# Performance work log

Measured on AMD Instinct MI355X. Metric: run time of the kernel, lower is better.

Reference implementation:

```python
import jax, jax.numpy as jnp
import numpy as np

H = 128      # hidden_size
B = 8192     # number of sessions
L = 50       # items per session (constant here; code supports ragged)
T = B * L    # total tokens


def setup_inputs() -> dict:
    key = jax.random.key(0)
    ks = jax.random.split(key, 10)
    s = 1.0 / np.sqrt(H)
    u = lambda k, shape: jax.random.uniform(k, shape, jnp.float32, -s, s)
    return {
        "intra_item_emb": jax.random.normal(ks[0], (T, H), jnp.float32),
        "inter_item_emb": jax.random.normal(ks[1], (T, H), jnp.float32),
        "W1": u(ks[2], (H, H)), "b1": u(ks[3], (H,)),
        "W2": u(ks[4], (H, H)), "b2": u(ks[5], (H,)),
        "q_w": u(ks[6], (1, H)), "q_b": u(ks[7], (1,)),
        "W3": u(ks[8], (H, 2 * H)), "b3": u(ks[9], (H,)),
        "seq_len": jnp.full((B,), L, dtype=jnp.int32),
    }


def reference(intra_item_emb, inter_item_emb, W1, b1, W2, b2, q_w, q_b, W3, b3, seq_len):
    # max_fusing: elementwise max of the two embedding streams  [T, H]
    hidden = jnp.maximum(intra_item_emb, inter_item_emb)
    nB = seq_len.shape[0]
    nT = hidden.shape[0]
    # segment id per token and index of last token of each session
    seg_ids = jnp.repeat(jnp.arange(nB), seq_len, total_repeat_length=nT)  # [T]
    last_idx = jnp.cumsum(seq_len) - 1                                      # [B]
    v_n = hidden[last_idx]                 # [B, H] last node of each session
    v_n_rep = v_n[seg_ids]                 # [T, H] broadcast last node to tokens
    # attention weight per token: q(sigmoid(W1 v_n + W2 h))  [T, 1]
    alpha = jax.nn.sigmoid(v_n_rep @ W1.T + b1 + hidden @ W2.T + b2) @ q_w.T + q_b
    # segment-sum pooling of alpha-weighted tokens  [B, H]
    s_g = jax.ops.segment_sum(alpha * hidden, seg_ids, num_segments=nB)
    # final session representation  [B, H]
    h_s = jnp.concatenate([v_n, s_g], axis=1) @ W3.T + b3
    return h_s
```

## Files before the change

kernel.cpp:

```cpp
#include <hip/hip_runtime.h>
#include <hip/hip_bf16.h>

#define HDIM 128
#define RS 136

typedef __attribute__((ext_vector_type(8))) short short8;
typedef __attribute__((ext_vector_type(4))) float floatv4;

static __device__ __forceinline__ unsigned short f2bf(float f) {
  union { float f; unsigned u; } x; x.f = f;
  unsigned r = x.u + 0x7fffu + ((x.u >> 16) & 1u);
  return (unsigned short)(r >> 16);
}
static __device__ __forceinline__ float blo(unsigned u) { return __uint_as_float(u << 16); }
static __device__ __forceinline__ float bhi(unsigned u) { return __uint_as_float(u & 0xffff0000u); }

__global__ void prep_kernel(const int* __restrict__ seq, int* __restrict__ offs, int B,
                            const float* __restrict__ W1, const float* __restrict__ W2,
                            const float* __restrict__ W3,
                            unsigned short* __restrict__ w1b, unsigned short* __restrict__ w2b,
                            unsigned short* __restrict__ w3b) {
  if (blockIdx.x == 0) {
    __shared__ int part[256];
    int tid = threadIdx.x;
    int chunk = (B + 255) >> 8;
    int beg = tid * chunk, end = min(beg + chunk, B);
    int s = 0;
    for (int i = beg; i < end; ++i) s += seq[i];
    part[tid] = s;
    __syncthreads();
    for (int d = 1; d < 256; d <<= 1) {
      int v = (tid >= d) ? part[tid - d] : 0;
      __syncthreads();
      part[tid] += v;
      __syncthreads();
    }
    int run = (tid == 0) ? 0 : part[tid - 1];
    for (int i = beg; i < end; ++i) { offs[i] = run; run += seq[i]; }
  } else {
    int i = (blockIdx.x - 1) * 256 + threadIdx.x;
    if (i < 16384) { w1b[i] = f2bf(W1[i]); w2b[i] = f2bf(W2[i]); }
    if (i < 32768) { w3b[i] = f2bf(W3[i]); }
  }
}

__global__ __launch_bounds__(256) void session_kernel(
    const float* __restrict__ intra, const float* __restrict__ inter,
    const unsigned short* __restrict__ w1b, const float* __restrict__ b1,
    const unsigned short* __restrict__ w2b, const float* __restrict__ b2,
    const float* __restrict__ qw, const float* __restrict__ qb,
    const unsigned short* __restrict__ w3b, const float* __restrict__ b3,
    const int* __restrict__ seq, const int* __restrict__ offs,
    float* __restrict__ out) {
  __shared__ unsigned short hbf[64 * RS];
  __shared__ unsigned short vnb[HDIM];
  __shared__ unsigned short sgb[HDIM];
  __shared__ float alphaAcc[64];
  __shared__ float sgpart[4][HDIM];

  const int b = blockIdx.x;
  const int tid = threadIdx.x;
  const int lane = tid & 63, wid = tid >> 6;
  const int quad = lane >> 4, lcol = lane & 15;
  const int nbase = wid << 5;
  const int n0 = nbase + lcol, n1 = n0 + 16;

  int n = seq[b];
  const int start = offs[b];
  if (n > 64) n = 64;

  if (tid < HDIM) {
    int last = start + n - 1;
    if (last < 0) last = 0;
    size_t base = (size_t)last * HDIM + tid;
    vnb[tid] = f2bf(fmaxf(intra[base], inter[base]));
  }
  if (tid < 64) alphaAcc[tid] = qb[0];

  {
    const float4* pa = (const float4*)(intra + (size_t)start * HDIM);
    const float4* pb = (const float4*)(inter + (size_t)start * HDIM);
    #pragma unroll
    for (int it = 0; it < 8; ++it) {
      int idx = (it << 8) + tid;
      int t = idx >> 5, j4 = idx & 31;
      float4 r; r.x = 0.f; r.y = 0.f; r.z = 0.f; r.w = 0.f;
      if (t < n) {
        float4 a = pa[idx], c = pb[idx];
        r.x = fmaxf(a.x, c.x); r.y = fmaxf(a.y, c.y);
        r.z = fmaxf(a.z, c.z); r.w = fmaxf(a.w, c.w);
      }
      union { __hip_bfloat162 b; unsigned u; } p01, p23;
      p01.b = __float22bfloat162_rn(make_float2(r.x, r.y));
      p23.b = __float22bfloat162_rn(make_float2(r.z, r.w));
      uint2 st; st.x = p01.u; st.y = p23.u;
      *(uint2*)&hbf[t * RS + (j4 << 2)] = st;
    }
  }

  short8 w2f[2][4];
  #pragma unroll
  for (int nt = 0; nt < 2; ++nt) {
    int nn = nbase + (nt << 4) + lcol;
    #pragma unroll
    for (int kt = 0; kt < 4; ++kt)
      w2f[nt][kt] = *(const short8*)(w2b + nn * HDIM + (kt << 5) + (quad << 3));
  }
  __syncthreads();

  float c0, c1;
  {
    floatv4 p0 = {0.f, 0.f, 0.f, 0.f}, p1 = {0.f, 0.f, 0.f, 0.f};
    #pragma unroll
    for (int kt = 0; kt < 4; ++kt) {
      short8 af = *(const short8*)&vnb[(kt << 5) + (quad << 3)];
      short8 bf0 = *(const short8*)(w1b + n0 * HDIM + (kt << 5) + (quad << 3));
      short8 bf1 = *(const short8*)(w1b + n1 * HDIM + (kt << 5) + (quad << 3));
      p0 = __builtin_amdgcn_mfma_f32_16x16x32_bf16(af, bf0, p0, 0, 0, 0);
      p1 = __builtin_amdgcn_mfma_f32_16x16x32_bf16(af, bf1, p1, 0, 0, 0);
    }
    c0 = p0[0] + b1[n0] + b2[n0];
    c1 = p1[0] + b1[n1] + b2[n1];
  }
  const float q0 = qw[n0], q1 = qw[n1];

  #pragma unroll
  for (int mt = 0; mt < 4; ++mt) {
    floatv4 a0 = {c0, c0, c0, c0}, a1 = {c1, c1, c1, c1};
    const unsigned short* arow = &hbf[((mt << 4) + lcol) * RS + (quad << 3)];
    #pragma unroll
    for (int kt = 0; kt < 4; ++kt) {
      short8 af = *(const short8*)(arow + (kt << 5));
      a0 = __builtin_amdgcn_mfma_f32_16x16x32_bf16(af, w2f[0][kt], a0, 0, 0, 0);
      a1 = __builtin_amdgcn_mfma_f32_16x16x32_bf16(af, w2f[1][kt], a1, 0, 0, 0);
    }
    #pragma unroll
    for (int r = 0; r < 4; ++r) {
      float v = q0 * __builtin_amdgcn_rcpf(1.f + __expf(-a0[r]))
              + q1 * __builtin_amdgcn_rcpf(1.f + __expf(-a1[r]));
      v += __shfl_xor(v, 1, 64);
      v += __shfl_xor(v, 2, 64);
      v += __shfl_xor(v, 4, 64);
      v += __shfl_xor(v, 8, 64);
      if (lcol == 0) atomicAdd(&alphaAcc[(mt << 4) + (quad << 2) + r], v);
    }
  }
  __syncthreads();

  {
    int jg = tid & 15, ts = tid >> 4;
    float ac[8];
    #pragma unroll
    for (int e = 0; e < 8; ++e) ac[e] = 0.f;
    #pragma unroll
    for (int tt = 0; tt < 4; ++tt) {
      int t = (tt << 4) + ts;
      float al = alphaAcc[t];
      uint4 u = *(const uint4*)&hbf[t * RS + (jg << 3)];
      ac[0] += al * blo(u.x); ac[1] += al * bhi(u.x);
      ac[2] += al * blo(u.y); ac[3] += al * bhi(u.y);
      ac[4] += al * blo(u.z); ac[5] += al * bhi(u.z);
      ac[6] += al * blo(u.w); ac[7] += al * bhi(u.w);
    }
    #pragma unroll
    for (int e = 0; e < 8; ++e) {
      ac[e] += __shfl_xor(ac[e], 16, 64);
      ac[e] += __shfl_xor(ac[e], 32, 64);
    }
    if (quad == 0) {
      float4 s0; s0.x = ac[0]; s0.y = ac[1]; s0.z = ac[2]; s0.w = ac[3];
      float4 s1; s1.x = ac[4]; s1.y = ac[5]; s1.z = ac[6]; s1.w = ac[7];
      *(float4*)&sgpart[wid][(jg << 3)] = s0;
      *(float4*)&sgpart[wid][(jg << 3) + 4] = s1;
    }
  }
  __syncthreads();
  if (tid < HDIM) {
    float s = sgpart[0][tid] + sgpart[1][tid] + sgpart[2][tid] + sgpart[3][tid];
    sgb[tid] = f2bf(s);
  }
  __syncthreads();

  {
    floatv4 o0 = {0.f, 0.f, 0.f, 0.f}, o1 = {0.f, 0.f, 0.f, 0.f};
    #pragma unroll
    for (int kt = 0; kt < 8; ++kt) {
      const unsigned short* src = (kt < 4) ? &vnb[kt << 5] : &sgb[(kt - 4) << 5];
      short8 af = *(const short8*)(src + (quad << 3));
      short8 bf0 = *(const short8*)(w3b + n0 * 256 + (kt << 5) + (quad << 3));
      short8 bf1 = *(const short8*)(w3b + n1 * 256 + (kt << 5) + (quad << 3));
      o0 = __builtin_amdgcn_mfma_f32_16x16x32_bf16(af, bf0, o0, 0, 0, 0);
      o1 = __builtin_amdgcn_mfma_f32_16x16x32_bf16(af, bf1, o1, 0, 0, 0);
    }
    if (quad == 0) {
      out[(size_t)b * HDIM + n0] = o0[0] + b3[n0];
      out[(size_t)b * HDIM + n1] = o1[0] + b3[n1];
    }
  }
}

extern "C" void kernel_launch(void* const* d_in, const int* in_sizes, int n_in,
                              void* d_out, int out_size, void* d_ws, size_t ws_size,
                              hipStream_t stream) {
  const float* intra = (const float*)d_in[0];
  const float* inter = (const float*)d_in[1];
  const float* W1 = (const float*)d_in[2];
  const float* b1 = (const float*)d_in[3];
  const float* W2 = (const float*)d_in[4];
  const float* b2 = (const float*)d_in[5];
  const float* qw = (const float*)d_in[6];
  const float* qb = (const float*)d_in[7];
  const float* W3 = (const float*)d_in[8];
  const float* b3 = (const float*)d_in[9];
  const int* seq = (const int*)d_in[10];
  const int B = in_sizes[10];
  float* out = (float*)d_out;

  char* ws = (char*)d_ws;
  size_t o1 = (((size_t)B * 4) + 255) & ~(size_t)255;
  int* offs = (int*)ws;
  unsigned short* w1b = (unsigned short*)(ws + o1);
  unsigned short* w2b = (unsigned short*)(ws + o1 + 32768);
  unsigned short* w3b = (unsigned short*)(ws + o1 + 65536);

  hipLaunchKernelGGL(prep_kernel, dim3(129), dim3(256), 0, stream,
                     seq, offs, B, W1, W2, W3, w1b, w2b, w3b);
  hipLaunchKernelGGL(session_kernel, dim3(B), dim3(256), 0, stream,
                     intra, inter, w1b, b1, w2b, b2, qw, qb, w3b, b3, seq, offs, out);
}
```

Baseline: 507.6 us.

## Process eight sessions per block with register-prefetched next session loads

Each block now handles eight sessions. The next session's embeddings are prefetched into registers while the current one is being processed, which overlaps global loads with MFMA work. The W1 and W3 projections are batched across the eight sessions into single MFMA tiles, where before each block used one useful row out of sixteen. W2 fragments are loaded once per block instead of once per session. The cost is heavy register use for the prefetch buffers (launch bounds set to 3 blocks), one eighth as many blocks, and more syncs per block.

```diff
diff --git a/kernel.cpp b/kernel.cpp
--- a/kernel.cpp
+++ b/kernel.cpp
@@ -3,6 +3,8 @@
 
 #define HDIM 128
 #define RS 136
+#define XS 264
+#define SPB 8
 
 typedef __attribute__((ext_vector_type(8))) short short8;
 typedef __attribute__((ext_vector_type(4))) float floatv4;
@@ -44,140 +46,184 @@
   }
 }
 
-__global__ __launch_bounds__(256) void session_kernel(
+__global__ __launch_bounds__(256, 3) void session_kernel(
     const float* __restrict__ intra, const float* __restrict__ inter,
     const unsigned short* __restrict__ w1b, const float* __restrict__ b1,
     const unsigned short* __restrict__ w2b, const float* __restrict__ b2,
     const float* __restrict__ qw, const float* __restrict__ qb,
     const unsigned short* __restrict__ w3b, const float* __restrict__ b3,
     const int* __restrict__ seq, const int* __restrict__ offs,
-    float* __restrict__ out) {
+    float* __restrict__ out, int B) {
   __shared__ unsigned short hbf[64 * RS];
-  __shared__ unsigned short vnb[HDIM];
-  __shared__ unsigned short sgb[HDIM];
-  __shared__ float alphaAcc[64];
+  __shared__ unsigned short X[16 * XS];
+  __shared__ float cbuf[SPB][HDIM];
+  __shared__ float alphaPart[4][64];
   __shared__ float sgpart[4][HDIM];
 
-  const int b = blockIdx.x;
   const int tid = threadIdx.x;
   const int lane = tid & 63, wid = tid >> 6;
   const int quad = lane >> 4, lcol = lane & 15;
-  const int nbase = wid << 5;
-  const int n0 = nbase + lcol, n1 = n0 + 16;
-
-  int n = seq[b];
-  const int start = offs[b];
-  if (n > 64) n = 64;
-
-  if (tid < HDIM) {
-    int last = start + n - 1;
-    if (last < 0) last = 0;
-    size_t base = (size_t)last * HDIM + tid;
-    vnb[tid] = f2bf(fmaxf(intra[base], inter[base]));
-  }
-  if (tid < 64) alphaAcc[tid] = qb[0];
-
+  const int n0 = (wid << 5) + lcol, n1 = n0 + 16;
+  const int sid0 = blockIdx.x * SPB;
+
+  int n_nxt = 0, start_nxt = 0;
+  if (sid0 < B) { n_nxt = seq[sid0]; start_nxt = offs[sid0]; }
+
+  float4 ra[8], rb[8];
   {
-    const float4* pa = (const float4*)(intra + (size_t)start * HDIM);
-    const float4* pb = (const float4*)(inter + (size_t)start * HDIM);
+    const float4* pa = (const float4*)(intra + (size_t)start_nxt * HDIM);
+    const float4* pb = (const float4*)(inter + (size_t)start_nxt * HDIM);
+    int nc = (n_nxt > 64) ? 64 : n_nxt;
     #pragma unroll
     for (int it = 0; it < 8; ++it) {
       int idx = (it << 8) + tid;
-      int t = idx >> 5, j4 = idx & 31;
-      float4 r; r.x = 0.f; r.y = 0.f; r.z = 0.f; r.w = 0.f;
-      if (t < n) {
-        float4 a = pa[idx], c = pb[idx];
-        r.x = fmaxf(a.x, c.x); r.y = fmaxf(a.y, c.y);
-        r.z = fmaxf(a.z, c.z); r.w = fmaxf(a.w, c.w);
-      }
-      union { __hip_bfloat162 b; unsigned u; } p01, p23;
-      p01.b = __float22bfloat162_rn(make_float2(r.x, r.y));
-      p23.b = __float22bfloat162_rn(make_float2(r.z, r.w));
-      uint2 st; st.x = p01.u; st.y = p23.u;
-      *(uint2*)&hbf[t * RS + (j4 << 2)] = st;
-    }
-  }
+      int t = idx >> 5;
+      float4 va = {0.f, 0.f, 0.f, 0.f}, vb = {0.f, 0.f, 0.f, 0.f};
+      if (t < nc) { va = pa[idx]; vb = pb[idx]; }
+      ra[it] = va; rb[it] = vb;
+    }
+  }
+  if (1 < SPB && sid0 + 1 < B) { n_nxt = seq[sid0 + 1]; start_nxt = offs[sid0 + 1]; }
+  else { n_nxt = 0; start_nxt = 0; }
 
   short8 w2f[2][4];
   #pragma unroll
   for (int nt = 0; nt < 2; ++nt) {
-    int nn = nbase + (nt << 4) + lcol;
+    int nn = n0 + (nt << 4);
     #pragma unroll
     for (int kt = 0; kt < 4; ++kt)
       w2f[nt][kt] = *(const short8*)(w2b + nn * HDIM + (kt << 5) + (quad << 3));
   }
+  const float q0 = qw[n0], q1 = qw[n1];
+  const float sq = qb[0];
+
+  #pragma unroll
+  for (int it = 0; it < 4; ++it) {
+    int s = (it << 1) + (tid >> 7);
+    int col = tid & 127;
+    int sid = sid0 + s;
+    int ns = 0, st = 0;
+    if (sid < B) { ns = seq[sid]; st = offs[sid]; }
+    float v = 0.f;
+    if (ns > 0) {
+      size_t base = (size_t)(st + ns - 1) * HDIM + col;
+      v = fmaxf(intra[base], inter[base]);
+    }
+    X[s * XS + col] = f2bf(v);
+  }
   __syncthreads();
 
-  float c0, c1;
   {
     floatv4 p0 = {0.f, 0.f, 0.f, 0.f}, p1 = {0.f, 0.f, 0.f, 0.f};
     #pragma unroll
     for (int kt = 0; kt < 4; ++kt) {
-      short8 af = *(const short8*)&vnb[(kt << 5) + (quad << 3)];
+      short8 af = *(const short8*)&X[lcol * XS + (kt << 5) + (quad << 3)];
       short8 bf0 = *(const short8*)(w1b + n0 * HDIM + (kt << 5) + (quad << 3));
       short8 bf1 = *(const short8*)(w1b + n1 * HDIM + (kt << 5) + (quad << 3));
       p0 = __builtin_amdgcn_mfma_f32_16x16x32_bf16(af, bf0, p0, 0, 0, 0);
       p1 = __builtin_amdgcn_mfma_f32_16x16x32_bf16(af, bf1, p1, 0, 0, 0);
     }
-    c0 = p0[0] + b1[n0] + b2[n0];
-    c1 = p1[0] + b1[n1] + b2[n1];
-  }
-  const float q0 = qw[n0], q1 = qw[n1];
-
-  #pragma unroll
-  for (int mt = 0; mt < 4; ++mt) {
-    floatv4 a0 = {c0, c0, c0, c0}, a1 = {c1, c1, c1, c1};
-    const unsigned short* arow = &hbf[((mt << 4) + lcol) * RS + (quad << 3)];
-    #pragma unroll
-    for (int kt = 0; kt < 4; ++kt) {
-      short8 af = *(const short8*)(arow + (kt << 5));
-      a0 = __builtin_amdgcn_mfma_f32_16x16x32_bf16(af, w2f[0][kt], a0, 0, 0, 0);
-      a1 = __builtin_amdgcn_mfma_f32_16x16x32_bf16(af, w2f[1][kt], a1, 0, 0, 0);
-    }
-    #pragma unroll
-    for (int r = 0; r < 4; ++r) {
-      float v = q0 * __builtin_amdgcn_rcpf(1.f + __expf(-a0[r]))
-              + q1 * __builtin_amdgcn_rcpf(1.f + __expf(-a1[r]));
-      v += __shfl_xor(v, 1, 64);
-      v += __shfl_xor(v, 2, 64);
-      v += __shfl_xor(v, 4, 64);
-      v += __shfl_xor(v, 8, 64);
-      if (lcol == 0) atomicAdd(&alphaAcc[(mt << 4) + (quad << 2) + r], v);
+    if (quad < 2) {
+      float bb0 = b1[n0] + b2[n0], bb1 = b1[n1] + b2[n1];
+      #pragma unroll
+      for (int r = 0; r < 4; ++r) {
+        int m = (quad << 2) + r;
+        cbuf[m][n0] = p0[r] + bb0;
+        cbuf[m][n1] = p1[r] + bb1;
+      }
     }
   }
   __syncthreads();
 
-  {
-    int jg = tid & 15, ts = tid >> 4;
-    float ac[8];
-    #pragma unroll
-    for (int e = 0; e < 8; ++e) ac[e] = 0.f;
-    #pragma unroll
-    for (int tt = 0; tt < 4; ++tt) {
-      int t = (tt << 4) + ts;
-      float al = alphaAcc[t];
-      uint4 u = *(const uint4*)&hbf[t * RS + (jg << 3)];
-      ac[0] += al * blo(u.x); ac[1] += al * bhi(u.x);
-      ac[2] += al * blo(u.y); ac[3] += al * bhi(u.y);
-      ac[4] += al * blo(u.z); ac[5] += al * bhi(u.z);
-      ac[6] += al * blo(u.w); ac[7] += al * bhi(u.w);
-    }
-    #pragma unroll
-    for (int e = 0; e < 8; ++e) {
-      ac[e] += __shfl_xor(ac[e], 16, 64);
-      ac[e] += __shfl_xor(ac[e], 32, 64);
-    }
-    if (quad == 0) {
-      float4 s0; s0.x = ac[0]; s0.y = ac[1]; s0.z = ac[2]; s0.w = ac[3];
-      float4 s1; s1.x = ac[4]; s1.y = ac[5]; s1.z = ac[6]; s1.w = ac[7];
-      *(float4*)&sgpart[wid][(jg << 3)] = s0;
-      *(float4*)&sgpart[wid][(jg << 3) + 4] = s1;
-    }
-  }
-  __syncthreads();
-  if (tid < HDIM) {
-    float s = sgpart[0][tid] + sgpart[1][tid] + sgpart[2][tid] + sgpart[3][tid];
-    sgb[tid] = f2bf(s);
+  #pragma unroll 1
+  for (int s = 0; s < SPB; ++s) {
+    #pragma unroll
+    for (int it = 0; it < 8; ++it) {
+      int idx = (it << 8) + tid;
+      int t = idx >> 5, j4 = idx & 31;
+      float4 a = ra[it], c = rb[it];
+      union { __hip_bfloat162 b; unsigned u; } p01, p23;
+      p01.b = __float22bfloat162_rn(make_float2(fmaxf(a.x, c.x), fmaxf(a.y, c.y)));
+      p23.b = __float22bfloat162_rn(make_float2(fmaxf(a.z, c.z), fmaxf(a.w, c.w)));
+      uint2 st; st.x = p01.u; st.y = p23.u;
+      *(uint2*)&hbf[t * RS + (j4 << 2)] = st;
+    }
+    __syncthreads();
+
+    if (s + 1 < SPB) {
+      const float4* pa = (const float4*)(intra + (size_t)start_nxt * HDIM);
+      const float4* pb = (const float4*)(inter + (size_t)start_nxt * HDIM);
+      int nc = (n_nxt > 64) ? 64 : n_nxt;
+      #pragma unroll
+      for (int it = 0; it < 8; ++it) {
+        int idx = (it << 8) + tid;
+        int t = idx >> 5;
+        float4 va = {0.f, 0.f, 0.f, 0.f}, vb = {0.f, 0.f, 0.f, 0.f};
+        if (t < nc) { va = pa[idx]; vb = pb[idx]; }
+        ra[it] = va; rb[it] = vb;
+      }
+    }
+    int n_n2 = 0, st_n2 = 0;
+    if (s + 2 < SPB && sid0 + s + 2 < B) { n_n2 = seq[sid0 + s + 2]; st_n2 = offs[sid0 + s + 2]; }
+
+    float c0 = cbuf[s][n0], c1 = cbuf[s][n1];
+    #pragma unroll
+    for (int mt = 0; mt < 4; ++mt) {
+      floatv4 a0 = {c0, c0, c0, c0}, a1 = {c1, c1, c1, c1};
+      const unsigned short* arow = &hbf[((mt << 4) + lcol) * RS + (quad << 3)];
+      #pragma unroll
+      for (int kt = 0; kt < 4; ++kt) {
+        short8 af = *(const short8*)(arow + (kt << 5));
+        a0 = __builtin_amdgcn_mfma_f32_16x16x32_bf16(af, w2f[0][kt], a0, 0, 0, 0);
+        a1 = __builtin_amdgcn_mfma_f32_16x16x32_bf16(af, w2f[1][kt], a1, 0, 0, 0);
+      }
+      #pragma unroll
+      for (int r = 0; r < 4; ++r) {
+        float v = q0 * __builtin_amdgcn_rcpf(1.f + __expf(-a0[r]))
+                + q1 * __builtin_amdgcn_rcpf(1.f + __expf(-a1[r]));
+        v += __shfl_xor(v, 1, 64);
+        v += __shfl_xor(v, 2, 64);
+        v += __shfl_xor(v, 4, 64);
+        v += __shfl_xor(v, 8, 64);
+        if (lcol == 0) alphaPart[wid][(mt << 4) + (quad << 2) + r] = v;
+      }
+    }
+    __syncthreads();
+
+    {
+      int jg = tid & 15, ts = tid >> 4;
+      float ac[8];
+      #pragma unroll
+      for (int e = 0; e < 8; ++e) ac[e] = 0.f;
+      #pragma unroll
+      for (int tt = 0; tt < 4; ++tt) {
+        int t = (tt << 4) + ts;
+        float al = sq + alphaPart[0][t] + alphaPart[1][t] + alphaPart[2][t] + alphaPart[3][t];
+        uint4 u = *(const uint4*)&hbf[t * RS + (jg << 3)];
+        ac[0] += al * blo(u.x); ac[1] += al * bhi(u.x);
+        ac[2] += al * blo(u.y); ac[3] += al * bhi(u.y);
+        ac[4] += al * blo(u.z); ac[5] += al * bhi(u.z);
+        ac[6] += al * blo(u.w); ac[7] += al * bhi(u.w);
+      }
+      #pragma unroll
+      for (int e = 0; e < 8; ++e) {
+        ac[e] += __shfl_xor(ac[e], 16, 64);
+        ac[e] += __shfl_xor(ac[e], 32, 64);
+      }
+      if (quad == 0) {
+        float4 s0; s0.x = ac[0]; s0.y = ac[1]; s0.z = ac[2]; s0.w = ac[3];
+        float4 s1; s1.x = ac[4]; s1.y = ac[5]; s1.z = ac[6]; s1.w = ac[7];
+        *(float4*)&sgpart[wid][(jg << 3)] = s0;
+        *(float4*)&sgpart[wid][(jg << 3) + 4] = s1;
+      }
+    }
+    __syncthreads();
+
+    if (tid < HDIM) {
+      float sgv = sgpart[0][tid] + sgpart[1][tid] + sgpart[2][tid] + sgpart[3][tid];
+      X[s * XS + HDIM + tid] = f2bf(sgv);
+    }
+    n_nxt = n_n2; start_nxt = st_n2;
   }
   __syncthreads();
 
@@ -185,16 +231,23 @@
     floatv4 o0 = {0.f, 0.f, 0.f, 0.f}, o1 = {0.f, 0.f, 0.f, 0.f};
     #pragma unroll
     for (int kt = 0; kt < 8; ++kt) {
-      const unsigned short* src = (kt < 4) ? &vnb[kt << 5] : &sgb[(kt - 4) << 5];
-      short8 af = *(const short8*)(src + (quad << 3));
+      short8 af = *(const short8*)&X[lcol * XS + (kt << 5) + (quad << 3)];
       short8 bf0 = *(const short8*)(w3b + n0 * 256 + (kt << 5) + (quad << 3));
       short8 bf1 = *(const short8*)(w3b + n1 * 256 + (kt << 5) + (quad << 3));
       o0 = __builtin_amdgcn_mfma_f32_16x16x32_bf16(af, bf0, o0, 0, 0, 0);
       o1 = __builtin_amdgcn_mfma_f32_16x16x32_bf16(af, bf1, o1, 0, 0, 0);
     }
-    if (quad == 0) {
-      out[(size_t)b * HDIM + n0] = o0[0] + b3[n0];
-      out[(size_t)b * HDIM + n1] = o1[0] + b3[n1];
+    if (quad < 2) {
+      float b30 = b3[n0], b31 = b3[n1];
+      #pragma unroll
+      for (int r = 0; r < 4; ++r) {
+        int m = (quad << 2) + r;
+        int sid = sid0 + m;
+        if (sid < B) {
+          out[(size_t)sid * HDIM + n0] = o0[r] + b30;
+          out[(size_t)sid * HDIM + n1] = o1[r] + b31;
+        }
+      }
     }
   }
 }
@@ -225,6 +278,7 @@
 
   hipLaunchKernelGGL(prep_kernel, dim3(129), dim3(256), 0, stream,
                      seq, offs, B, W1, W2, W3, w1b, w2b, w3b);
-  hipLaunchKernelGGL(session_kernel, dim3(B), dim3(256), 0, stream,
-                     intra, inter, w1b, b1, w2b, b2, qw, qb, w3b, b3, seq, offs, out);
-}
+  int nblk = (B + SPB - 1) / SPB;
+  hipLaunchKernelGGL(session_kernel, dim3(nblk), dim3(256), 0, stream,
+                     intra, inter, w1b, b1, w2b, b2, qw, qb, w3b, b3, seq, offs, out, B);
+}
```

Measured after the change: 542.3 us. 1.07x slower.
